# Kernel tuning notes

Hardware: AMD Instinct MI355X
Metric: run time of the kernel (lower is better)

Reference implementation:

```python
import jax, jax.numpy as jnp
import numpy as np

MAP_SIZE = 56
K_STEEP = 10.0  # boxcar sigmoid steepness (the 'k=10' default in the original)


def setup_inputs() -> dict:
    key = jax.random.key(0)
    k1, k2, k3 = jax.random.split(key, 3)
    B, D, H = 16384, 1024, 512
    x = jax.random.normal(k1, (B, D), dtype=jnp.float32)
    W1 = jax.random.normal(k2, (D, H), dtype=jnp.float32) * (1.0 / np.sqrt(D))
    b1 = jnp.zeros((H,), dtype=jnp.float32)
    W2 = jax.random.normal(k3, (H, 3), dtype=jnp.float32) * (1.0 / np.sqrt(H))
    b2 = jnp.zeros((3,), dtype=jnp.float32)
    return {"x": x, "W1": W1, "b1": b1, "W2": W2, "b2": b2}


def boxcar(t, map_size=MAP_SIZE, k=K_STEEP):
    # t: [B, 3] = (x_center, y_center, size). Vectorized over batch and grid.
    t0 = t[:, 0][:, None, None]  # [B,1,1]
    t1 = t[:, 1][:, None, None]
    t2 = t[:, 2][:, None, None]
    i = jnp.arange(map_size, dtype=t.dtype)[None, :, None]  # [1,S,1]
    j = jnp.arange(map_size, dtype=t.dtype)[None, None, :]  # [1,1,S]
    Vx = jax.nn.sigmoid(k * (i - t0 + 0.5 * t2)) - jax.nn.sigmoid(k * (i - t0 - 0.5 * t2))
    Vy = jax.nn.sigmoid(k * (j - t1 + 0.5 * t2)) - jax.nn.sigmoid(k * (j - t1 - 0.5 * t2))
    return Vx * Vy  # [B,S,S]


def reference(x, W1, b1, W2, b2):
    # fc1 -> fc2 (flatten output is discarded in the original call(), as in source)
    h = x @ W1 + b1          # [B, hidden]
    t = h @ W2 + b2          # [B, 3]
    return boxcar(t)         # [B, map_size, map_size]
```

## Files before the change

### kernel.cpp

```cpp
#include <hip/hip_runtime.h>
#include <math.h>

#define MAP 56
#define KST 10.0f
#define BATCH 16384
#define DIM 1024
#define HID 512

__global__ __launch_bounds__(64) void fold_weights(
    const float* __restrict__ W1, const float* __restrict__ b1,
    const float* __restrict__ W2, const float* __restrict__ b2,
    float* __restrict__ Weff, float* __restrict__ beff)
{
    const int d = blockIdx.x;
    const int lane = threadIdx.x;
    const float* row = (d < DIM) ? (W1 + (size_t)d * HID) : b1;

    float a0 = 0.f, a1 = 0.f, a2 = 0.f;
    for (int h = lane; h < HID; h += 64) {
        float w = row[h];
        const float* w2 = W2 + h * 3;
        a0 += w * w2[0];
        a1 += w * w2[1];
        a2 += w * w2[2];
    }
    #pragma unroll
    for (int off = 32; off; off >>= 1) {
        a0 += __shfl_down(a0, off, 64);
        a1 += __shfl_down(a1, off, 64);
        a2 += __shfl_down(a2, off, 64);
    }
    if (lane == 0) {
        if (d < DIM) {
            Weff[d * 3 + 0] = a0;
            Weff[d * 3 + 1] = a1;
            Weff[d * 3 + 2] = a2;
        } else {
            beff[0] = a0 + b2[0];
            beff[1] = a1 + b2[1];
            beff[2] = a2 + b2[2];
        }
    }
}

__global__ __launch_bounds__(256) void boxcar_kernel(
    const float* __restrict__ x, const float* __restrict__ Weff,
    const float* __restrict__ beff, float* __restrict__ out)
{
    __shared__ float sV[2][MAP];
    __shared__ float sred[4][3];
    __shared__ float st[3];

    const int b = blockIdx.x;
    const int tid = threadIdx.x;

    const float4 xv = ((const float4*)(x + (size_t)b * DIM))[tid];
    const float* wp = Weff + (tid * 4) * 3;
    float a0 = xv.x * wp[0] + xv.y * wp[3] + xv.z * wp[6] + xv.w * wp[9];
    float a1 = xv.x * wp[1] + xv.y * wp[4] + xv.z * wp[7] + xv.w * wp[10];
    float a2 = xv.x * wp[2] + xv.y * wp[5] + xv.z * wp[8] + xv.w * wp[11];
    #pragma unroll
    for (int off = 32; off; off >>= 1) {
        a0 += __shfl_down(a0, off, 64);
        a1 += __shfl_down(a1, off, 64);
        a2 += __shfl_down(a2, off, 64);
    }
    const int wave = tid >> 6;
    if ((tid & 63) == 0) {
        sred[wave][0] = a0; sred[wave][1] = a1; sred[wave][2] = a2;
    }
    __syncthreads();
    if (tid == 0) {
        st[0] = sred[0][0] + sred[1][0] + sred[2][0] + sred[3][0] + beff[0];
        st[1] = sred[0][1] + sred[1][1] + sred[2][1] + sred[3][1] + beff[1];
        st[2] = sred[0][2] + sred[1][2] + sred[2][2] + sred[3][2] + beff[2];
    }
    __syncthreads();
    const float t0 = st[0], t1 = st[1], t2 = st[2];

    if (tid < 128) {
        const int which = tid >> 6;
        const int i = tid & 63;
        if (i < MAP) {
            const float tc = which ? t1 : t0;
            const float u = (float)i - tc;
            const float hh = 0.5f * t2;
            const float p = 1.0f / (1.0f + __expf(-KST * (u + hh)));
            const float m = 1.0f / (1.0f + __expf(-KST * (u - hh)));
            sV[which][i] = p - m;
        }
    }
    __syncthreads();

    float4* ob = (float4*)(out + (size_t)b * (MAP * MAP));
    for (int idx = tid; idx < (MAP * MAP / 4); idx += 256) {
        const int i = idx / (MAP / 4);
        const int jq = idx - i * (MAP / 4);
        const float vx = sV[0][i];
        float4 o;
        o.x = vx * sV[1][4 * jq + 0];
        o.y = vx * sV[1][4 * jq + 1];
        o.z = vx * sV[1][4 * jq + 2];
        o.w = vx * sV[1][4 * jq + 3];
        ob[idx] = o;
    }
}

extern "C" void kernel_launch(void* const* d_in, const int* in_sizes, int n_in,
                              void* d_out, int out_size, void* d_ws, size_t ws_size,
                              hipStream_t stream) {
    const float* x  = (const float*)d_in[0];
    const float* W1 = (const float*)d_in[1];
    const float* b1 = (const float*)d_in[2];
    const float* W2 = (const float*)d_in[3];
    const float* b2 = (const float*)d_in[4];
    float* out = (float*)d_out;

    float* Weff = (float*)d_ws;
    float* beff = Weff + DIM * 3;

    fold_weights<<<DIM + 1, 64, 0, stream>>>(W1, b1, W2, b2, Weff, beff);
    boxcar_kernel<<<BATCH, 256, 0, stream>>>(x, Weff, beff, out);
}
```

Baseline: 265.7 us.

## Split GEMV from boxcar expansion and batch multiple rows per block

Splits the fused per-row kernel into a GEMV kernel and a boxcar kernel. The GEMV kernel processes four rows per wave with the folded weights, transposed, held in registers. The boxcar kernel expands eight rows per block and reads precomputed [B,3] parameters, reusing a float4 shared layout. The goal is to remove the per-row block synchronisation and reduction overhead and make the large output write more streaming-friendly, at the cost of an extra launch and an intermediate buffer.

After: 273.1 us. 2.8% more time.

```diff
diff --git a/kernel.cpp b/kernel.cpp
--- a/kernel.cpp
+++ b/kernel.cpp
@@ -6,11 +6,13 @@
 #define BATCH 16384
 #define DIM 1024
 #define HID 512
+#define RPB 8
+#define RPW 4
 
 __global__ __launch_bounds__(64) void fold_weights(
     const float* __restrict__ W1, const float* __restrict__ b1,
     const float* __restrict__ W2, const float* __restrict__ b2,
-    float* __restrict__ Weff, float* __restrict__ beff)
+    float* __restrict__ WeffT, float* __restrict__ beff)
 {
     const int d = blockIdx.x;
     const int lane = threadIdx.x;
@@ -18,11 +20,10 @@
 
     float a0 = 0.f, a1 = 0.f, a2 = 0.f;
     for (int h = lane; h < HID; h += 64) {
-        float w = row[h];
-        const float* w2 = W2 + h * 3;
-        a0 += w * w2[0];
-        a1 += w * w2[1];
-        a2 += w * w2[2];
+        const float w = row[h];
+        a0 += w * W2[h * 3 + 0];
+        a1 += w * W2[h * 3 + 1];
+        a2 += w * W2[h * 3 + 2];
     }
     #pragma unroll
     for (int off = 32; off; off >>= 1) {
@@ -32,9 +33,9 @@
     }
     if (lane == 0) {
         if (d < DIM) {
-            Weff[d * 3 + 0] = a0;
-            Weff[d * 3 + 1] = a1;
-            Weff[d * 3 + 2] = a2;
+            WeffT[0 * DIM + d] = a0;
+            WeffT[1 * DIM + d] = a1;
+            WeffT[2 * DIM + d] = a2;
         } else {
             beff[0] = a0 + b2[0];
             beff[1] = a1 + b2[1];
@@ -43,66 +44,88 @@
     }
 }
 
+__global__ __launch_bounds__(256) void gemv_kernel(
+    const float* __restrict__ x, const float* __restrict__ WeffT,
+    const float* __restrict__ beff, float4* __restrict__ t4)
+{
+    const int tid  = threadIdx.x;
+    const int wave = tid >> 6;
+    const int lane = tid & 63;
+    const int row0 = blockIdx.x * (4 * RPW) + wave * RPW;
+
+    float4 wf[3][4];
+    #pragma unroll
+    for (int q = 0; q < 4; ++q)
+        #pragma unroll
+        for (int c = 0; c < 3; ++c)
+            wf[c][q] = *(const float4*)(WeffT + c * DIM + 4 * lane + 256 * q);
+
+    float acc[RPW][3];
+    #pragma unroll
+    for (int r = 0; r < RPW; ++r) { acc[r][0] = acc[r][1] = acc[r][2] = 0.f; }
+
+    #pragma unroll
+    for (int r = 0; r < RPW; ++r) {
+        const float* xr = x + (size_t)(row0 + r) * DIM;
+        #pragma unroll
+        for (int q = 0; q < 4; ++q) {
+            const float4 xv = *(const float4*)(xr + 4 * lane + 256 * q);
+            acc[r][0] += xv.x * wf[0][q].x + xv.y * wf[0][q].y + xv.z * wf[0][q].z + xv.w * wf[0][q].w;
+            acc[r][1] += xv.x * wf[1][q].x + xv.y * wf[1][q].y + xv.z * wf[1][q].z + xv.w * wf[1][q].w;
+            acc[r][2] += xv.x * wf[2][q].x + xv.y * wf[2][q].y + xv.z * wf[2][q].z + xv.w * wf[2][q].w;
+        }
+    }
+    #pragma unroll
+    for (int off = 32; off; off >>= 1)
+        #pragma unroll
+        for (int r = 0; r < RPW; ++r) {
+            acc[r][0] += __shfl_down(acc[r][0], off, 64);
+            acc[r][1] += __shfl_down(acc[r][1], off, 64);
+            acc[r][2] += __shfl_down(acc[r][2], off, 64);
+        }
+    if (lane == 0) {
+        const float b0 = beff[0], b1 = beff[1], b2 = beff[2];
+        #pragma unroll
+        for (int r = 0; r < RPW; ++r)
+            t4[row0 + r] = make_float4(acc[r][0] + b0, acc[r][1] + b1, acc[r][2] + b2, 0.f);
+    }
+}
+
 __global__ __launch_bounds__(256) void boxcar_kernel(
-    const float* __restrict__ x, const float* __restrict__ Weff,
-    const float* __restrict__ beff, float* __restrict__ out)
+    const float4* __restrict__ t4, float* __restrict__ out)
 {
-    __shared__ float sV[2][MAP];
-    __shared__ float sred[4][3];
-    __shared__ float st[3];
+    __shared__ float  sVx[RPB][MAP];
+    __shared__ float4 sVy4[RPB][MAP / 4];
 
-    const int b = blockIdx.x;
-    const int tid = threadIdx.x;
+    const int tid  = threadIdx.x;
+    const int base = blockIdx.x * RPB;
 
-    const float4 xv = ((const float4*)(x + (size_t)b * DIM))[tid];
-    const float* wp = Weff + (tid * 4) * 3;
-    float a0 = xv.x * wp[0] + xv.y * wp[3] + xv.z * wp[6] + xv.w * wp[9];
-    float a1 = xv.x * wp[1] + xv.y * wp[4] + xv.z * wp[7] + xv.w * wp[10];
-    float a2 = xv.x * wp[2] + xv.y * wp[5] + xv.z * wp[8] + xv.w * wp[11];
-    #pragma unroll
-    for (int off = 32; off; off >>= 1) {
-        a0 += __shfl_down(a0, off, 64);
-        a1 += __shfl_down(a1, off, 64);
-        a2 += __shfl_down(a2, off, 64);
-    }
-    const int wave = tid >> 6;
-    if ((tid & 63) == 0) {
-        sred[wave][0] = a0; sred[wave][1] = a1; sred[wave][2] = a2;
-    }
-    __syncthreads();
-    if (tid == 0) {
-        st[0] = sred[0][0] + sred[1][0] + sred[2][0] + sred[3][0] + beff[0];
-        st[1] = sred[0][1] + sred[1][1] + sred[2][1] + sred[3][1] + beff[1];
-        st[2] = sred[0][2] + sred[1][2] + sred[2][2] + sred[3][2] + beff[2];
-    }
-    __syncthreads();
-    const float t0 = st[0], t1 = st[1], t2 = st[2];
-
-    if (tid < 128) {
-        const int which = tid >> 6;
-        const int i = tid & 63;
-        if (i < MAP) {
-            const float tc = which ? t1 : t0;
-            const float u = (float)i - tc;
-            const float hh = 0.5f * t2;
-            const float p = 1.0f / (1.0f + __expf(-KST * (u + hh)));
-            const float m = 1.0f / (1.0f + __expf(-KST * (u - hh)));
-            sV[which][i] = p - m;
-        }
+    for (int e = tid; e < RPB * 2 * MAP; e += 256) {
+        const int sub = e / (2 * MAP);
+        const int ent = e - sub * (2 * MAP);
+        const float4 t = t4[base + sub];
+        const int  isY = ent >= MAP;
+        const int  i   = isY ? ent - MAP : ent;
+        const float tc = isY ? t.y : t.x;
+        const float u  = (float)i - tc;
+        const float hh = 0.5f * t.z;
+        const float p  = 1.0f / (1.0f + __expf(-KST * (u + hh)));
+        const float m  = 1.0f / (1.0f + __expf(-KST * (u - hh)));
+        const float v  = p - m;
+        if (isY) ((float*)&sVy4[sub][0])[i] = v;
+        else     sVx[sub][i] = v;
     }
     __syncthreads();
 
-    float4* ob = (float4*)(out + (size_t)b * (MAP * MAP));
-    for (int idx = tid; idx < (MAP * MAP / 4); idx += 256) {
-        const int i = idx / (MAP / 4);
-        const int jq = idx - i * (MAP / 4);
-        const float vx = sV[0][i];
-        float4 o;
-        o.x = vx * sV[1][4 * jq + 0];
-        o.y = vx * sV[1][4 * jq + 1];
-        o.z = vx * sV[1][4 * jq + 2];
-        o.w = vx * sV[1][4 * jq + 3];
-        ob[idx] = o;
+    float4* ob = (float4*)(out + (size_t)base * (MAP * MAP));
+    for (int g = tid; g < RPB * (MAP * MAP / 4); g += 256) {
+        const int sub = g / (MAP * MAP / 4);
+        const int rem = g - sub * (MAP * MAP / 4);
+        const int i   = rem / (MAP / 4);
+        const int jq  = rem - i * (MAP / 4);
+        const float  vx = sVx[sub][i];
+        const float4 vy = sVy4[sub][jq];
+        ob[g] = make_float4(vx * vy.x, vx * vy.y, vx * vy.z, vx * vy.w);
     }
 }
 
@@ -116,9 +139,11 @@
     const float* b2 = (const float*)d_in[4];
     float* out = (float*)d_out;
 
-    float* Weff = (float*)d_ws;
-    float* beff = Weff + DIM * 3;
+    float*  WeffT = (float*)d_ws;
+    float*  beff  = WeffT + 3 * DIM;
+    float4* t4    = (float4*)(beff + 4);
 
-    fold_weights<<<DIM + 1, 64, 0, stream>>>(W1, b1, W2, b2, Weff, beff);
-    boxcar_kernel<<<BATCH, 256, 0, stream>>>(x, Weff, beff, out);
+    fold_weights<<<DIM + 1, 64, 0, stream>>>(W1, b1, W2, b2, WeffT, beff);
+    gemv_kernel<<<BATCH / (4 * RPW), 256, 0, stream>>>(x, WeffT, beff, t4);
+    boxcar_kernel<<<BATCH / RPB, 256, 0, stream>>>(t4, out);
 }
```
